# Kernel tuning notes

Hardware: AMD Instinct MI355X
Metric: run time of the kernel (lower is better)

The kernel has to match this reference:

```python
import jax, jax.numpy as jnp
import numpy as np

D_MODEL = 2048
N_EXPERTS = 64
TOP_K = 8
N_TOKENS = 16384


def setup_inputs() -> dict:
    key = jax.random.key(0)
    k1, k2 = jax.random.split(key)
    x_flat = jax.random.normal(k1, (N_TOKENS, D_MODEL), dtype=jnp.float32)
    # nn.Linear(d_model, n_experts) weight has shape [n_experts, d_model]
    gate_w = jax.random.normal(k2, (N_EXPERTS, D_MODEL), dtype=jnp.float32) * (1.0 / np.sqrt(D_MODEL))
    return {"x_flat": x_flat, "gate_w": gate_w}


def reference(x_flat, gate_w):
    # logits = x_flat @ gate_w.T : [tokens, n_experts]
    logits = jnp.einsum("td,ed->te", x_flat, gate_w)
    full_probs = jax.nn.softmax(logits, axis=-1)
    topk_logits, topk_idx = jax.lax.top_k(logits, TOP_K)
    topk_weights = jax.nn.softmax(topk_logits, axis=-1)
    return topk_idx, topk_weights, full_probs, logits
```

## Files before the change

kernel.cpp:

```cpp
#include <hip/hip_runtime.h>
#include <math.h>

#define D_MODEL   2048
#define N_EXPERTS 64
#define TOP_K     8
#define N_TOKENS  16384
#define NTHREADS  256
#define WS_NEED   (64*4*3*64*16)

typedef __attribute__((ext_vector_type(8))) short bf16x8;
typedef __attribute__((ext_vector_type(4))) float f32x4;
typedef __attribute__((ext_vector_type(4))) int   i32x4;

union FragU { i32x4 i; bf16x8 h; };

__device__ __forceinline__ void split3(float x, unsigned &h, unsigned &m, unsigned &l) {
    unsigned ux = __float_as_uint(x);
    h = ux & 0xffff0000u;
    float mf = x - __uint_as_float(h);
    unsigned um = __float_as_uint(mf) & 0xffff0000u;
    float lf = mf - __uint_as_float(um);
    m = um;
    l = __float_as_uint(lf) & 0xffff0000u;
}

__global__ __launch_bounds__(256) void pack_w_kernel(const float* __restrict__ gw,
                                                     unsigned* __restrict__ wp) {
    const int g    = blockIdx.x * 256 + threadIdx.x;
    const int d    = g & 3;
    const int lane = (g >> 2) & 63;
    const int rest = g >> 8;
    const int v    = rest % 3;
    const int t    = rest / 3;
    const int fr   = t & 3;
    const int ks   = t >> 2;
    const int e    = fr * 16 + (lane & 15);
    const int k    = ks * 32 + (lane >> 4) * 8 + 2 * d;
    const float w0 = gw[(size_t)e * D_MODEL + k];
    const float w1 = gw[(size_t)e * D_MODEL + k + 1];
    unsigned h0, m0, l0, h1, m1, l1;
    split3(w0, h0, m0, l0);
    split3(w1, h1, m1, l1);
    const unsigned c0 = (v == 0) ? h0 : ((v == 1) ? m0 : l0);
    const unsigned c1 = (v == 0) ? h1 : ((v == 1) ? m1 : l1);
    wp[g] = (c0 >> 16) | c1;
}

__device__ __forceinline__ void splitpack(const float4 a, const float4 b,
                                          FragU &ph, FragU &pm, FragU &pl) {
    const float f[8] = {a.x, a.y, a.z, a.w, b.x, b.y, b.z, b.w};
#pragma unroll
    for (int d = 0; d < 4; ++d) {
        unsigned h0, m0, l0, h1, m1, l1;
        split3(f[2 * d],     h0, m0, l0);
        split3(f[2 * d + 1], h1, m1, l1);
        ph.i[d] = (int)((h0 >> 16) | h1);
        pm.i[d] = (int)((m0 >> 16) | m1);
        pl.i[d] = (int)((l0 >> 16) | l1);
    }
}

#define MFMA(A_, B_, C_) C_ = __builtin_amdgcn_mfma_f32_16x16x32_bf16((A_).h, (B_).h, C_, 0, 0, 0)

#define FRAG6(Bh_, Bm_, Bl_, ACCA_, ACCB_)                                   \
    {                                                                        \
        FragU bh_, bm_, bl_;                                                 \
        bh_.i = Bh_; bm_.i = Bm_; bl_.i = Bl_;                               \
        MFMA(ah, bh_, ACCA_); MFMA(am_, bh_, ACCA_); MFMA(al, bh_, ACCA_);   \
        MFMA(ah, bm_, ACCB_); MFMA(am_, bm_, ACCB_); MFMA(ah, bl_, ACCB_);   \
    }

__global__ __launch_bounds__(NTHREADS, 4) void router_mfma(
    const float* __restrict__ x, const unsigned* __restrict__ wp,
    float* __restrict__ out)
{
    __shared__ __align__(16) float part[4 * 1088 + 32];

    const int tid  = threadIdx.x;
    const int lane = tid & 63;
    const int q    = tid >> 6;
    const int m0   = blockIdx.x * 16;

    const int lrow = lane & 15;
    const int lk   = lane >> 4;

    const float* xa = x + (size_t)(m0 + lrow) * D_MODEL + q * 512 + lk * 8;
    const unsigned* wb = wp + (size_t)q * 49152 + lane * 4;

    f32x4 acc0a = {0.f,0.f,0.f,0.f}, acc0b = acc0a;
    f32x4 acc1a = acc0a, acc1b = acc0a;
    f32x4 acc2a = acc0a, acc2b = acc0a;
    f32x4 acc3a = acc0a, acc3b = acc0a;

    float4 Aa = *(const float4*)(xa);
    float4 Ab = *(const float4*)(xa + 4);

#pragma unroll 2
    for (int s = 0; s < 16; ++s) {
        const unsigned* bt = wb + s * 3072;
        const i32x4 B0h = *(const i32x4*)(bt +    0);
        const i32x4 B0m = *(const i32x4*)(bt +  256);
        const i32x4 B0l = *(const i32x4*)(bt +  512);
        const i32x4 B1h = *(const i32x4*)(bt +  768);
        const i32x4 B1m = *(const i32x4*)(bt + 1024);
        const i32x4 B1l = *(const i32x4*)(bt + 1280);
        const i32x4 B2h = *(const i32x4*)(bt + 1536);
        const i32x4 B2m = *(const i32x4*)(bt + 1792);
        const i32x4 B2l = *(const i32x4*)(bt + 2048);
        const i32x4 B3h = *(const i32x4*)(bt + 2304);
        const i32x4 B3m = *(const i32x4*)(bt + 2560);
        const i32x4 B3l = *(const i32x4*)(bt + 2816);

        float4 Na = Aa, Nb = Ab;
        if (s + 1 < 16) {
            Na = *(const float4*)(xa + (s + 1) * 32);
            Nb = *(const float4*)(xa + (s + 1) * 32 + 4);
        }

        FragU ah, am_, al;
        splitpack(Aa, Ab, ah, am_, al);

        FRAG6(B0h, B0m, B0l, acc0a, acc0b);
        FRAG6(B1h, B1m, B1l, acc1a, acc1b);
        FRAG6(B2h, B2m, B2l, acc2a, acc2b);
        FRAG6(B3h, B3m, B3l, acc3a, acc3b);

        Aa = Na; Ab = Nb;
    }

    {
        float* ps = part + q * 1088;
#pragma unroll
        for (int reg = 0; reg < 4; ++reg) {
            const int tok = lk * 4 + reg;
            ps[tok * 68 +  0 + lrow] = acc0a[reg] + acc0b[reg];
            ps[tok * 68 + 16 + lrow] = acc1a[reg] + acc1b[reg];
            ps[tok * 68 + 32 + lrow] = acc2a[reg] + acc2b[reg];
            ps[tok * 68 + 48 + lrow] = acc3a[reg] + acc3b[reg];
        }
    }
    __syncthreads();

    {
        const int tok = tid >> 4;
        const int e0  = (tid & 15) * 4;
        const int o   = tok * 68 + e0;
        float4 s0 = *(const float4*)(part + 0 * 1088 + o);
        float4 s1 = *(const float4*)(part + 1 * 1088 + o);
        float4 s2 = *(const float4*)(part + 2 * 1088 + o);
        float4 s3 = *(const float4*)(part + 3 * 1088 + o);
        float4 r = make_float4(s0.x + s1.x + s2.x + s3.x,
                               s0.y + s1.y + s2.y + s3.y,
                               s0.z + s1.z + s2.z + s3.z,
                               s0.w + s1.w + s2.w + s3.w);
        *(float4*)(part + o) = r;
    }
    __syncthreads();

    float* lt   = part;
    float* smax = part + 4 * 1088;
    float* srs  = smax + 16;

    float* out_idx = out;
    float* out_w   = out + (size_t)N_TOKENS * TOP_K;
    float* out_p   = out + (size_t)2 * N_TOKENS * TOP_K;
    float* out_l   = out_p + (size_t)N_TOKENS * N_EXPERTS;

    if (tid < 16) {
        const int t = tid;
        float tv[TOP_K];
        int   ti[TOP_K];
#pragma unroll
        for (int i = 0; i < TOP_K; ++i) { tv[i] = -INFINITY; ti[i] = 0; }
        float m = -INFINITY;

        for (int e = 0; e < N_EXPERTS; ++e) {
            const float v = lt[t * 68 + e];
            m = fmaxf(m, v);
            if (v > tv[TOP_K - 1]) {
#pragma unroll
                for (int j = TOP_K - 1; j >= 1; --j) {
                    const bool shift = (v > tv[j - 1]);
                    const bool here  = (v > tv[j]);
                    const float ntv = shift ? tv[j - 1] : (here ? v : tv[j]);
                    const int   nti = shift ? ti[j - 1] : (here ? e : ti[j]);
                    tv[j] = ntv; ti[j] = nti;
                }
                if (v > tv[0]) { tv[0] = v; ti[0] = e; }
            }
        }

        float s = 0.f;
        for (int e = 0; e < N_EXPERTS; ++e) s += expf(lt[t * 68 + e] - m);
        const float rs = 1.f / s;
        smax[t] = m;
        srs[t]  = rs;

        float ex[TOP_K];
        float wsum = 0.f;
#pragma unroll
        for (int i = 0; i < TOP_K; ++i) { ex[i] = expf(tv[i] - tv[0]); wsum += ex[i]; }
        const float rw = 1.f / wsum;

        const int tok = m0 + t;
#pragma unroll
        for (int i = 0; i < TOP_K; ++i) {
            out_idx[(size_t)tok * TOP_K + i] = (float)ti[i];
            out_w  [(size_t)tok * TOP_K + i] = ex[i] * rw;
        }
    }
    __syncthreads();

    {
        const int f = tid * 4;
        const int t = f >> 6;
        const int e = f & 63;
        const float l0 = lt[t * 68 + e + 0];
        const float l1 = lt[t * 68 + e + 1];
        const float l2 = lt[t * 68 + e + 2];
        const float l3 = lt[t * 68 + e + 3];
        const float mm = smax[t];
        const float rr = srs[t];
        float4 pv = make_float4(expf(l0 - mm) * rr, expf(l1 - mm) * rr,
                                expf(l2 - mm) * rr, expf(l3 - mm) * rr);
        float4 lv = make_float4(l0, l1, l2, l3);
        const size_t gbase = (size_t)m0 * N_EXPERTS + f;
        *(float4*)(out_p + gbase) = pv;
        *(float4*)(out_l + gbase) = lv;
    }
}

__global__ __launch_bounds__(512) void router_fallback(
    const float* __restrict__ x, const float* __restrict__ gw,
    float* __restrict__ out)
{
    __shared__ float xs[64][33];
    __shared__ float wsh[N_EXPERTS][36];
    __shared__ float lt[64][N_EXPERTS + 1];
    __shared__ float smax[64], srs[64];

    const int tid  = threadIdx.x;
    const int lane = tid & 63;
    const int wv   = tid >> 6;
    const int m0   = blockIdx.x * 64;
    const int srow = tid >> 3;
    const int skq  = (tid & 7) * 4;

    const float* xsrc = x  + (size_t)(m0 + srow) * D_MODEL + skq;
    const float* wsrc = gw + (size_t)srow        * D_MODEL + skq;
    float4 xr = *(const float4*)(xsrc);
    float4 wr = *(const float4*)(wsrc);

    float acc[8];
#pragma unroll
    for (int i = 0; i < 8; ++i) acc[i] = 0.f;
    const int e0 = wv * 8;

    for (int c = 0; c < D_MODEL / 32; ++c) {
        xs[srow][skq] = xr.x; xs[srow][skq+1] = xr.y; xs[srow][skq+2] = xr.z; xs[srow][skq+3] = xr.w;
        *(float4*)&wsh[srow][skq] = wr;
        __syncthreads();
        if (c + 1 < D_MODEL / 32) {
            xr = *(const float4*)(xsrc + (c + 1) * 32);
            wr = *(const float4*)(wsrc + (c + 1) * 32);
        }
#pragma unroll 8
        for (int k4 = 0; k4 < 8; ++k4) {
            const float4 xv = *(const float4*)&xs[lane][k4 * 4];
#pragma unroll
            for (int e = 0; e < 8; ++e) {
                const float4 w4 = *(const float4*)&wsh[e0 + e][k4 * 4];
                acc[e] = fmaf(xv.x, w4.x, fmaf(xv.y, w4.y, fmaf(xv.z, w4.z, fmaf(xv.w, w4.w, acc[e]))));
            }
        }
        __syncthreads();
    }
#pragma unroll
    for (int e = 0; e < 8; ++e) lt[lane][e0 + e] = acc[e];
    __syncthreads();

    float* out_idx = out;
    float* out_w   = out + (size_t)N_TOKENS * TOP_K;
    float* out_p   = out + (size_t)2 * N_TOKENS * TOP_K;
    float* out_l   = out_p + (size_t)N_TOKENS * N_EXPERTS;

    if (tid < 64) {
        const int t = tid;
        float tv[TOP_K]; int ti[TOP_K];
#pragma unroll
        for (int i = 0; i < TOP_K; ++i) { tv[i] = -INFINITY; ti[i] = 0; }
        float m = -INFINITY;
        for (int e = 0; e < N_EXPERTS; ++e) {
            const float v = lt[t][e];
            m = fmaxf(m, v);
            if (v > tv[TOP_K - 1]) {
#pragma unroll
                for (int j = TOP_K - 1; j >= 1; --j) {
                    const bool shift = (v > tv[j - 1]);
                    const bool here  = (v > tv[j]);
                    const float ntv = shift ? tv[j - 1] : (here ? v : tv[j]);
                    const int   nti = shift ? ti[j - 1] : (here ? e : ti[j]);
                    tv[j] = ntv; ti[j] = nti;
                }
                if (v > tv[0]) { tv[0] = v; ti[0] = e; }
            }
        }
        float s = 0.f;
        for (int e = 0; e < N_EXPERTS; ++e) s += expf(lt[t][e] - m);
        const float rs = 1.f / s;
        smax[t] = m; srs[t] = rs;
        float ex[TOP_K]; float wsum = 0.f;
#pragma unroll
        for (int i = 0; i < TOP_K; ++i) { ex[i] = expf(tv[i] - tv[0]); wsum += ex[i]; }
        const float rw = 1.f / wsum;
        const int tok = m0 + t;
#pragma unroll
        for (int i = 0; i < TOP_K; ++i) {
            out_idx[(size_t)tok * TOP_K + i] = (float)ti[i];
            out_w  [(size_t)tok * TOP_K + i] = ex[i] * rw;
        }
    }
    __syncthreads();
#pragma unroll
    for (int rep = 0; rep < 2; ++rep) {
        const int f = rep * (512 * 4) + tid * 4;
        const int t = f >> 6;
        const int e = f & 63;
        const float l0 = lt[t][e], l1 = lt[t][e+1], l2 = lt[t][e+2], l3 = lt[t][e+3];
        const float mm = smax[t], rr = srs[t];
        float4 pv = make_float4(expf(l0-mm)*rr, expf(l1-mm)*rr, expf(l2-mm)*rr, expf(l3-mm)*rr);
        float4 lv = make_float4(l0, l1, l2, l3);
        const size_t gbase = (size_t)m0 * N_EXPERTS + f;
        *(float4*)(out_p + gbase) = pv;
        *(float4*)(out_l + gbase) = lv;
    }
}

extern "C" void kernel_launch(void* const* d_in, const int* in_sizes, int n_in,
                              void* d_out, int out_size, void* d_ws, size_t ws_size,
                              hipStream_t stream) {
    const float* x  = (const float*)d_in[0];
    const float* gw = (const float*)d_in[1];
    float* out = (float*)d_out;
    if (ws_size >= (size_t)WS_NEED) {
        unsigned* wp = (unsigned*)d_ws;
        pack_w_kernel<<<dim3(WS_NEED / 4 / 256), dim3(256), 0, stream>>>(gw, wp);
        router_mfma<<<dim3(N_TOKENS / 16), dim3(NTHREADS), 0, stream>>>(x, wp, out);
    } else {
        router_fallback<<<dim3(N_TOKENS / 64), dim3(512), 0, stream>>>(x, gw, out);
    }
}
```

Measured before the change: 81.78 us.

## Split router GEMM work by expert half and K half with double-buffered loads

Each 64-thread wave now handles 32 experts over half of the K dimension, where before it handled all 64 experts over a quarter of K. The K-reduction across waves shrinks from four partial sums to two, and shared memory use drops. The main loop is rewritten with explicit two-stage register double buffering of the B fragments and x loads, with sched_barrier fences to keep loads overlapping the MFMAs. The trade-off is that each wave must split its A fragments twice as often per MFMA, and the manual scheduling may constrain the compiler.

```diff
diff --git a/kernel.cpp b/kernel.cpp
--- a/kernel.cpp
+++ b/kernel.cpp
@@ -62,81 +62,98 @@
 
 #define MFMA(A_, B_, C_) C_ = __builtin_amdgcn_mfma_f32_16x16x32_bf16((A_).h, (B_).h, C_, 0, 0, 0)
 
-#define FRAG6(Bh_, Bm_, Bl_, ACCA_, ACCB_)                                   \
-    {                                                                        \
-        FragU bh_, bm_, bl_;                                                 \
-        bh_.i = Bh_; bm_.i = Bm_; bl_.i = Bl_;                               \
-        MFMA(ah, bh_, ACCA_); MFMA(am_, bh_, ACCA_); MFMA(al, bh_, ACCA_);   \
-        MFMA(ah, bm_, ACCB_); MFMA(am_, bm_, ACCB_); MFMA(ah, bl_, ACCB_);   \
-    }
-
 __global__ __launch_bounds__(NTHREADS, 4) void router_mfma(
     const float* __restrict__ x, const unsigned* __restrict__ wp,
     float* __restrict__ out)
 {
-    __shared__ __align__(16) float part[4 * 1088 + 32];
+    __shared__ __align__(16) float part[2 * 1088 + 32];
 
     const int tid  = threadIdx.x;
     const int lane = tid & 63;
     const int q    = tid >> 6;
+    const int eh   = q & 1;
+    const int kh   = q >> 1;
     const int m0   = blockIdx.x * 16;
 
     const int lrow = lane & 15;
     const int lk   = lane >> 4;
 
-    const float* xa = x + (size_t)(m0 + lrow) * D_MODEL + q * 512 + lk * 8;
-    const unsigned* wb = wp + (size_t)q * 49152 + lane * 4;
+    const float* xa = x + (size_t)(m0 + lrow) * D_MODEL + kh * 1024 + lk * 8;
+    const unsigned* wb = wp + (size_t)kh * 32 * 3072 + eh * 1536 + lane * 4;
 
     f32x4 acc0a = {0.f,0.f,0.f,0.f}, acc0b = acc0a;
     f32x4 acc1a = acc0a, acc1b = acc0a;
-    f32x4 acc2a = acc0a, acc2b = acc0a;
-    f32x4 acc3a = acc0a, acc3b = acc0a;
-
-    float4 Aa = *(const float4*)(xa);
-    float4 Ab = *(const float4*)(xa + 4);
-
-#pragma unroll 2
-    for (int s = 0; s < 16; ++s) {
-        const unsigned* bt = wb + s * 3072;
-        const i32x4 B0h = *(const i32x4*)(bt +    0);
-        const i32x4 B0m = *(const i32x4*)(bt +  256);
-        const i32x4 B0l = *(const i32x4*)(bt +  512);
-        const i32x4 B1h = *(const i32x4*)(bt +  768);
-        const i32x4 B1m = *(const i32x4*)(bt + 1024);
-        const i32x4 B1l = *(const i32x4*)(bt + 1280);
-        const i32x4 B2h = *(const i32x4*)(bt + 1536);
-        const i32x4 B2m = *(const i32x4*)(bt + 1792);
-        const i32x4 B2l = *(const i32x4*)(bt + 2048);
-        const i32x4 B3h = *(const i32x4*)(bt + 2304);
-        const i32x4 B3m = *(const i32x4*)(bt + 2560);
-        const i32x4 B3l = *(const i32x4*)(bt + 2816);
-
-        float4 Na = Aa, Nb = Ab;
-        if (s + 1 < 16) {
-            Na = *(const float4*)(xa + (s + 1) * 32);
-            Nb = *(const float4*)(xa + (s + 1) * 32 + 4);
-        }
-
-        FragU ah, am_, al;
-        splitpack(Aa, Ab, ah, am_, al);
-
-        FRAG6(B0h, B0m, B0l, acc0a, acc0b);
-        FRAG6(B1h, B1m, B1l, acc1a, acc1b);
-        FRAG6(B2h, B2m, B2l, acc2a, acc2b);
-        FRAG6(B3h, B3m, B3l, acc3a, acc3b);
-
-        Aa = Na; Ab = Nb;
-    }
+
+    i32x4 B0h, B0m, B0l, B1h, B1m, B1l;
+    i32x4 C0h, C0m, C0l, C1h, C1m, C1l;
+    float4 Aa0, Ab0, Aa1, Ab1;
+
+#define LOADB(s_, H0,M0,L0,H1,M1,L1)                                         \
+    {   const unsigned* bt_ = wb + (size_t)(s_) * 3072;                      \
+        H0 = *(const i32x4*)(bt_ +    0);                                    \
+        M0 = *(const i32x4*)(bt_ +  256);                                    \
+        L0 = *(const i32x4*)(bt_ +  512);                                    \
+        H1 = *(const i32x4*)(bt_ +  768);                                    \
+        M1 = *(const i32x4*)(bt_ + 1024);                                    \
+        L1 = *(const i32x4*)(bt_ + 1280); }
+
+    LOADB(0, B0h,B0m,B0l,B1h,B1m,B1l);
+    Aa0 = *(const float4*)(xa);
+    Ab0 = *(const float4*)(xa + 4);
+    LOADB(1, C0h,C0m,C0l,C1h,C1m,C1l);
+    Aa1 = *(const float4*)(xa + 32);
+    Ab1 = *(const float4*)(xa + 36);
+    __builtin_amdgcn_sched_barrier(0);
+
+    for (int s = 0; s < 32; s += 2) {
+        {
+            FragU ah, am_, al;
+            splitpack(Aa0, Ab0, ah, am_, al);
+            FragU bh, bm, bl, ch, cm, cl;
+            bh.i = B0h; bm.i = B0m; bl.i = B0l;
+            ch.i = B1h; cm.i = B1m; cl.i = B1l;
+            MFMA(ah, bh, acc0a);  MFMA(ah, ch, acc1a);
+            MFMA(am_, bh, acc0a); MFMA(am_, ch, acc1a);
+            MFMA(al, bh, acc0a);  MFMA(al, ch, acc1a);
+            MFMA(ah, bm, acc0b);  MFMA(ah, cm, acc1b);
+            MFMA(am_, bm, acc0b); MFMA(am_, cm, acc1b);
+            MFMA(ah, bl, acc0b);  MFMA(ah, cl, acc1b);
+            if (s < 30) {
+                LOADB(s + 2, B0h,B0m,B0l,B1h,B1m,B1l);
+                Aa0 = *(const float4*)(xa + (s + 2) * 32);
+                Ab0 = *(const float4*)(xa + (s + 2) * 32 + 4);
+            }
+            __builtin_amdgcn_sched_barrier(0);
+        }
+        {
+            FragU ah, am_, al;
+            splitpack(Aa1, Ab1, ah, am_, al);
+            FragU bh, bm, bl, ch, cm, cl;
+            bh.i = C0h; bm.i = C0m; bl.i = C0l;
+            ch.i = C1h; cm.i = C1m; cl.i = C1l;
+            MFMA(ah, bh, acc0a);  MFMA(ah, ch, acc1a);
+            MFMA(am_, bh, acc0a); MFMA(am_, ch, acc1a);
+            MFMA(al, bh, acc0a);  MFMA(al, ch, acc1a);
+            MFMA(ah, bm, acc0b);  MFMA(ah, cm, acc1b);
+            MFMA(am_, bm, acc0b); MFMA(am_, cm, acc1b);
+            MFMA(ah, bl, acc0b);  MFMA(ah, cl, acc1b);
+            if (s < 30) {
+                LOADB(s + 3, C0h,C0m,C0l,C1h,C1m,C1l);
+                Aa1 = *(const float4*)(xa + (s + 3) * 32);
+                Ab1 = *(const float4*)(xa + (s + 3) * 32 + 4);
+            }
+            __builtin_amdgcn_sched_barrier(0);
+        }
+    }
+#undef LOADB
 
     {
-        float* ps = part + q * 1088;
+        float* ps = part + kh * 1088;
 #pragma unroll
         for (int reg = 0; reg < 4; ++reg) {
             const int tok = lk * 4 + reg;
-            ps[tok * 68 +  0 + lrow] = acc0a[reg] + acc0b[reg];
-            ps[tok * 68 + 16 + lrow] = acc1a[reg] + acc1b[reg];
-            ps[tok * 68 + 32 + lrow] = acc2a[reg] + acc2b[reg];
-            ps[tok * 68 + 48 + lrow] = acc3a[reg] + acc3b[reg];
+            ps[tok * 68 + eh * 32 +  0 + lrow] = acc0a[reg] + acc0b[reg];
+            ps[tok * 68 + eh * 32 + 16 + lrow] = acc1a[reg] + acc1b[reg];
         }
     }
     __syncthreads();
@@ -145,20 +162,16 @@
         const int tok = tid >> 4;
         const int e0  = (tid & 15) * 4;
         const int o   = tok * 68 + e0;
-        float4 s0 = *(const float4*)(part + 0 * 1088 + o);
-        float4 s1 = *(const float4*)(part + 1 * 1088 + o);
-        float4 s2 = *(const float4*)(part + 2 * 1088 + o);
-        float4 s3 = *(const float4*)(part + 3 * 1088 + o);
-        float4 r = make_float4(s0.x + s1.x + s2.x + s3.x,
-                               s0.y + s1.y + s2.y + s3.y,
-                               s0.z + s1.z + s2.z + s3.z,
-                               s0.w + s1.w + s2.w + s3.w);
+        float4 s0 = *(const float4*)(part + o);
+        float4 s1 = *(const float4*)(part + 1088 + o);
+        float4 r = make_float4(s0.x + s1.x, s0.y + s1.y,
+                               s0.z + s1.z, s0.w + s1.w);
         *(float4*)(part + o) = r;
     }
     __syncthreads();
 
     float* lt   = part;
-    float* smax = part + 4 * 1088;
+    float* smax = part + 2 * 1088;
     float* srs  = smax + 16;
 
     float* out_idx = out;
```

Result: slower. 91.99 us (+12.5%).

## Split router GEMM across 8 waves by expert quarter and K half

Applied to the files above, without the earlier changes.

Doubles the block to 512 threads. Each wave now owns one 16-expert slice and half of the K dimension, where before each wave owned all 64 experts over a quarter of K. This cuts per-wave accumulator and B-fragment register pressure and allows higher occupancy (launch bound 8). In exchange, every wave redundantly loads and splits the same A tile for its K half, and the cross-wave reduction drops from four partial buffers to two.

```diff
diff --git a/kernel.cpp b/kernel.cpp
--- a/kernel.cpp
+++ b/kernel.cpp
@@ -5,7 +5,7 @@
 #define N_EXPERTS 64
 #define TOP_K     8
 #define N_TOKENS  16384
-#define NTHREADS  256
+#define NTHREADS  512
 #define WS_NEED   (64*4*3*64*16)
 
 typedef __attribute__((ext_vector_type(8))) short bf16x8;
@@ -62,103 +62,78 @@
 
 #define MFMA(A_, B_, C_) C_ = __builtin_amdgcn_mfma_f32_16x16x32_bf16((A_).h, (B_).h, C_, 0, 0, 0)
 
-#define FRAG6(Bh_, Bm_, Bl_, ACCA_, ACCB_)                                   \
-    {                                                                        \
-        FragU bh_, bm_, bl_;                                                 \
-        bh_.i = Bh_; bm_.i = Bm_; bl_.i = Bl_;                               \
-        MFMA(ah, bh_, ACCA_); MFMA(am_, bh_, ACCA_); MFMA(al, bh_, ACCA_);   \
-        MFMA(ah, bm_, ACCB_); MFMA(am_, bm_, ACCB_); MFMA(ah, bl_, ACCB_);   \
-    }
-
-__global__ __launch_bounds__(NTHREADS, 4) void router_mfma(
+__global__ __launch_bounds__(NTHREADS, 8) void router_mfma(
     const float* __restrict__ x, const unsigned* __restrict__ wp,
     float* __restrict__ out)
 {
-    __shared__ __align__(16) float part[4 * 1088 + 32];
+    __shared__ __align__(16) float part[2 * 1088 + 32];
 
     const int tid  = threadIdx.x;
     const int lane = tid & 63;
-    const int q    = tid >> 6;
+    const int w    = tid >> 6;
+    const int eh   = w & 3;
+    const int kh   = w >> 2;
     const int m0   = blockIdx.x * 16;
 
     const int lrow = lane & 15;
     const int lk   = lane >> 4;
 
-    const float* xa = x + (size_t)(m0 + lrow) * D_MODEL + q * 512 + lk * 8;
-    const unsigned* wb = wp + (size_t)q * 49152 + lane * 4;
-
-    f32x4 acc0a = {0.f,0.f,0.f,0.f}, acc0b = acc0a;
-    f32x4 acc1a = acc0a, acc1b = acc0a;
-    f32x4 acc2a = acc0a, acc2b = acc0a;
-    f32x4 acc3a = acc0a, acc3b = acc0a;
+    const float* xa = x + (size_t)(m0 + lrow) * D_MODEL + kh * 1024 + lk * 8;
+    const unsigned* wb = wp + (size_t)kh * 32 * 3072 + eh * 768 + lane * 4;
+
+    f32x4 accA = {0.f, 0.f, 0.f, 0.f};
+    f32x4 accB = accA;
 
     float4 Aa = *(const float4*)(xa);
     float4 Ab = *(const float4*)(xa + 4);
 
-#pragma unroll 2
-    for (int s = 0; s < 16; ++s) {
-        const unsigned* bt = wb + s * 3072;
-        const i32x4 B0h = *(const i32x4*)(bt +    0);
-        const i32x4 B0m = *(const i32x4*)(bt +  256);
-        const i32x4 B0l = *(const i32x4*)(bt +  512);
-        const i32x4 B1h = *(const i32x4*)(bt +  768);
-        const i32x4 B1m = *(const i32x4*)(bt + 1024);
-        const i32x4 B1l = *(const i32x4*)(bt + 1280);
-        const i32x4 B2h = *(const i32x4*)(bt + 1536);
-        const i32x4 B2m = *(const i32x4*)(bt + 1792);
-        const i32x4 B2l = *(const i32x4*)(bt + 2048);
-        const i32x4 B3h = *(const i32x4*)(bt + 2304);
-        const i32x4 B3m = *(const i32x4*)(bt + 2560);
-        const i32x4 B3l = *(const i32x4*)(bt + 2816);
+    for (int s = 0; s < 32; ++s) {
+        const unsigned* bt = wb + (size_t)s * 3072;
+        const i32x4 Bh = *(const i32x4*)(bt +   0);
+        const i32x4 Bm = *(const i32x4*)(bt + 256);
+        const i32x4 Bl = *(const i32x4*)(bt + 512);
 
         float4 Na = Aa, Nb = Ab;
-        if (s + 1 < 16) {
+        if (s + 1 < 32) {
             Na = *(const float4*)(xa + (s + 1) * 32);
             Nb = *(const float4*)(xa + (s + 1) * 32 + 4);
         }
 
         FragU ah, am_, al;
         splitpack(Aa, Ab, ah, am_, al);
-
-        FRAG6(B0h, B0m, B0l, acc0a, acc0b);
-        FRAG6(B1h, B1m, B1l, acc1a, acc1b);
-        FRAG6(B2h, B2m, B2l, acc2a, acc2b);
-        FRAG6(B3h, B3m, B3l, acc3a, acc3b);
+        FragU bh, bm, bl;
+        bh.i = Bh; bm.i = Bm; bl.i = Bl;
+
+        MFMA(ah, bh, accA);
+        MFMA(am_, bh, accA);
+        MFMA(al, bh, accA);
+        MFMA(ah, bm, accB);
+        MFMA(am_, bm, accB);
+        MFMA(ah, bl, accB);
 
         Aa = Na; Ab = Nb;
     }
 
     {
-        float* ps = part + q * 1088;
-#pragma unroll
-        for (int reg = 0; reg < 4; ++reg) {
-            const int tok = lk * 4 + reg;
-            ps[tok * 68 +  0 + lrow] = acc0a[reg] + acc0b[reg];
-            ps[tok * 68 + 16 + lrow] = acc1a[reg] + acc1b[reg];
-            ps[tok * 68 + 32 + lrow] = acc2a[reg] + acc2b[reg];
-            ps[tok * 68 + 48 + lrow] = acc3a[reg] + acc3b[reg];
-        }
-    }
-    __syncthreads();
-
-    {
-        const int tok = tid >> 4;
-        const int e0  = (tid & 15) * 4;
-        const int o   = tok * 68 + e0;
-        float4 s0 = *(const float4*)(part + 0 * 1088 + o);
-        float4 s1 = *(const float4*)(part + 1 * 1088 + o);
-        float4 s2 = *(const float4*)(part + 2 * 1088 + o);
-        float4 s3 = *(const float4*)(part + 3 * 1088 + o);
-        float4 r = make_float4(s0.x + s1.x + s2.x + s3.x,
-                               s0.y + s1.y + s2.y + s3.y,
-                               s0.z + s1.z + s2.z + s3.z,
-                               s0.w + s1.w + s2.w + s3.w);
+        float* ps = part + kh * 1088;
+#pragma unroll
+        for (int reg = 0; reg < 4; ++reg)
+            ps[(lk * 4 + reg) * 68 + eh * 16 + lrow] = accA[reg] + accB[reg];
+    }
+    __syncthreads();
+
+    if (tid < 256) {
+        const int o = (tid >> 4) * 68 + (tid & 15) * 4;
+        float4 s0 = *(const float4*)(part + o);
+        float4 s1 = *(const float4*)(part + 1088 + o);
+        float4 r = make_float4(s0.x + s1.x, s0.y + s1.y,
+                               s0.z + s1.z, s0.w + s1.w);
         *(float4*)(part + o) = r;
     }
     __syncthreads();
 
     float* lt   = part;
-    float* smax = part + 4 * 1088;
+    float* smax = part + 2 * 1088;
     float* srs  = smax + 16;
 
     float* out_idx = out;
@@ -211,7 +186,7 @@
     }
     __syncthreads();
 
-    {
+    if (tid < 256) {
         const int f = tid * 4;
         const int t = f >> 6;
         const int e = f & 63;
```

After: 118.2 us. 1.44x slower.
